# Kernel optimization log

Hardware: AMD Instinct MI355X
Metric: run time of the kernel (lower is better)

The kernel has to match this reference:

```python
import jax, jax.numpy as jnp
import numpy as np

HID = 128
N_NODES = 50000
N_EDGES = 640000
N_GRAPHS = 64
N_LAYERS = 3
LN_EPS = 1e-5


def _ln(h, g, b):
    mu = jnp.mean(h, axis=-1, keepdims=True)
    v = jnp.mean(jnp.square(h - mu), axis=-1, keepdims=True)
    return (h - mu) * jax.lax.rsqrt(v + LN_EPS) * g + b


def _mlp2(h, W1, b1, g, be, W2, b2):
    # Linear -> ReLU -> LayerNorm -> (Dropout=identity in eval) -> Linear
    h = _ln(jax.nn.relu(h @ W1.T + b1), g, be)
    return h @ W2.T + b2


def _forward(x, edge_index, batch, axis_W1, axis_b1, axis_g, axis_be, axis_W2, axis_b2, org_W1, org_b1, org_g, org_be, org_W2, org_b2, nin_W, nin_b, conv_W1, conv_b1, conv_g, conv_be, conv_W2, conv_b2, eps, ln_g, ln_b, gate_W1, gate_b1, gate_g, gate_be, gate_W2, gate_b2, head_W1, head_b1, head_g, head_be, head_W2, head_b2):
    axis = x[:, 9:12]
    origin = x[:, 12:15]
    others = jnp.concatenate([x[:, :9], x[:, 15:19]], axis=1)  # [N, 13]
    axis_z = _mlp2(axis, axis_W1, axis_b1, axis_g, axis_be, axis_W2, axis_b2)
    org_z = _mlp2(origin, org_W1, org_b1, org_g, org_be, org_W2, org_b2)
    h = jnp.concatenate([others, axis_z, org_z], axis=1) @ nin_W.T + nin_b  # [N, HID]
    src, dst = edge_index[0], edge_index[1]
    n = x.shape[0]
    for l in range(N_LAYERS):
        res = h
        # GIN: sum-aggregate source features into targets (gather + scatter-add)
        agg = jax.ops.segment_sum(h[src], dst, num_segments=n)
        m = (1.0 + eps[l]) * h + agg
        m = _mlp2(m, conv_W1[l], conv_b1[l], conv_g[l], conv_be[l], conv_W2[l], conv_b2[l])
        h = _ln(jax.nn.relu(m), ln_g[l], ln_b[l]) + res
    # AttentionalAggregation: segment softmax over per-graph node gates
    gate = _mlp2(h, gate_W1, gate_b1, gate_g, gate_be, gate_W2, gate_b2)  # [N, 1]
    gmax = jax.ops.segment_max(gate, batch, num_segments=N_GRAPHS)
    e = jnp.exp(gate - gmax[batch])
    denom = jax.ops.segment_sum(e, batch, num_segments=N_GRAPHS)
    attn = e / denom[batch]
    g = jax.ops.segment_sum(attn * h, batch, num_segments=N_GRAPHS)  # [B, HID]
    logit = _mlp2(g, head_W1, head_b1, head_g, head_be, head_W2, head_b2)[:, 0]
    return logit


def setup_inputs() -> dict:
    key = jax.random.key(0)
    ks = iter(jax.random.split(key, 64))
    nk = lambda: next(ks)
    lin = lambda o, i: jax.random.normal(nk(), (o, i), jnp.float32) / np.float32(np.sqrt(i))
    lin3 = lambda L, o, i: jnp.stack([lin(o, i) for _ in range(L)])
    z = lambda *s: jnp.zeros(s, jnp.float32)
    o = lambda *s: jnp.ones(s, jnp.float32)
    inp = {}
    inp['x'] = jax.random.normal(nk(), (N_NODES, 19), jnp.float32)
    inp['edge_index'] = jax.random.randint(nk(), (2, N_EDGES), 0, N_NODES)
    inp['batch'] = jnp.sort(jax.random.randint(nk(), (N_NODES,), 0, N_GRAPHS))
    for p in ('axis', 'org'):
        inp[p + '_W1'] = lin(16, 3); inp[p + '_b1'] = z(16)
        inp[p + '_g'] = o(16); inp[p + '_be'] = z(16)
        inp[p + '_W2'] = lin(16, 16); inp[p + '_b2'] = z(16)
    inp['nin_W'] = lin(HID, 45); inp['nin_b'] = z(HID)
    inp['conv_W1'] = lin3(N_LAYERS, HID, HID); inp['conv_b1'] = z(N_LAYERS, HID)
    inp['conv_g'] = o(N_LAYERS, HID); inp['conv_be'] = z(N_LAYERS, HID)
    inp['conv_W2'] = lin3(N_LAYERS, HID, HID); inp['conv_b2'] = z(N_LAYERS, HID)
    inp['eps'] = z(N_LAYERS)
    inp['ln_g'] = o(N_LAYERS, HID); inp['ln_b'] = z(N_LAYERS, HID)
    for p in ('gate', 'head'):
        inp[p + '_W1'] = lin(HID // 2, HID); inp[p + '_b1'] = z(HID // 2)
        inp[p + '_g'] = o(HID // 2); inp[p + '_be'] = z(HID // 2)
        inp[p + '_W2'] = lin(1, HID // 2); inp[p + '_b2'] = z(1)
    return inp


def reference(x, edge_index, batch, axis_W1, axis_b1, axis_g, axis_be, axis_W2, axis_b2, org_W1, org_b1, org_g, org_be, org_W2, org_b2, nin_W, nin_b, conv_W1, conv_b1, conv_g, conv_be, conv_W2, conv_b2, eps, ln_g, ln_b, gate_W1, gate_b1, gate_g, gate_be, gate_W2, gate_b2, head_W1, head_b1, head_g, head_be, head_W2, head_b2):
    return _forward(x, edge_index, batch, axis_W1, axis_b1, axis_g, axis_be, axis_W2, axis_b2, org_W1, org_b1, org_g, org_be, org_W2, org_b2, nin_W, nin_b, conv_W1, conv_b1, conv_g, conv_be, conv_W2, conv_b2, eps, ln_g, ln_b, gate_W1, gate_b1, gate_g, gate_be, gate_W2, gate_b2, head_W1, head_b1, head_g, head_be, head_W2, head_b2)
```

## Files before the change

### kernel.cpp

```cpp
#include <hip/hip_runtime.h>

#define N_NODESC 50000
#define N_EDGESC 640000
#define N_GRAPHSC 64
#define HIDC 128
#define LN_EPSF 1e-5f
#define POOL_SPLIT 16
#define SCAN_NB 49
#define EGRID ((N_EDGESC + 255) / 256)
#define NGRID_GB ((N_NODESC + 255) / 256)
#define NGRID64 ((N_NODESC + 63) / 64)
#define PREP_ELEMS (8192 + 49152 + 49152)
#define WPREP_NB ((PREP_ELEMS + 255) / 256)

typedef short bf16x8 __attribute__((ext_vector_type(8)));
typedef float f32x4 __attribute__((ext_vector_type(4)));

static __device__ __forceinline__ unsigned ord_enc(float f) {
  unsigned u = __float_as_uint(f);
  return (u & 0x80000000u) ? ~u : (u | 0x80000000u);
}
static __device__ __forceinline__ float ord_dec(unsigned u) {
  return __uint_as_float((u & 0x80000000u) ? (u ^ 0x80000000u) : ~u);
}
static __device__ __forceinline__ unsigned short f2bf(float x) {
  unsigned u = __float_as_uint(x);
  u += 0x7fffu + ((u >> 16) & 1u);
  return (unsigned short)(u >> 16);
}
static __device__ __forceinline__ float bf2f(unsigned short b) {
  return __uint_as_float(((unsigned)b) << 16);
}

static __device__ __forceinline__ void mlp16(float in0, float in1, float in2,
    const float* __restrict__ W1, const float* __restrict__ b1,
    const float* __restrict__ g, const float* __restrict__ be,
    const float* __restrict__ W2, const float* __restrict__ b2,
    float* __restrict__ out) {
  float h[16];
  float s1 = 0.f, s2 = 0.f;
#pragma unroll
  for (int j = 0; j < 16; ++j) {
    float v = b1[j] + W1[j*3+0]*in0 + W1[j*3+1]*in1 + W1[j*3+2]*in2;
    v = fmaxf(v, 0.f);
    h[j] = v; s1 += v; s2 += v*v;
  }
  float mu = s1 * (1.f/16.f);
  float var = fmaxf(s2 * (1.f/16.f) - mu*mu, 0.f);
  float rs = rsqrtf(var + LN_EPSF);
  float z[16];
#pragma unroll
  for (int j = 0; j < 16; ++j) z[j] = (h[j]-mu)*rs*g[j] + be[j];
#pragma unroll
  for (int j = 0; j < 16; ++j) {
    float v = b2[j];
#pragma unroll
    for (int k = 0; k < 16; ++k) v += W2[j*16+k]*z[k];
    out[j] = v;
  }
}

__global__ __launch_bounds__(256) void hist_gbound_kernel(const int* __restrict__ ei,
    int* __restrict__ deg, const int* __restrict__ batch, int* __restrict__ gstart,
    const float* __restrict__ ninW, unsigned short* __restrict__ ninWb,
    const float* __restrict__ cW1, unsigned short* __restrict__ cW1b,
    const float* __restrict__ cW2, unsigned short* __restrict__ cW2b) {
  const int b = blockIdx.x;
  if (b < EGRID) {
    int e = b * 256 + threadIdx.x;
    if (e < N_EDGESC) atomicAdd(&deg[ei[N_EDGESC + e]], 1);
  } else if (b < EGRID + NGRID_GB) {
    int i = (b - EGRID) * 256 + threadIdx.x;
    if (i >= N_NODESC) return;
    int bb = batch[i];
    int prev = (i == 0) ? -1 : batch[i-1];
    for (int g = prev + 1; g <= bb; ++g) gstart[g] = i;
    if (i == N_NODESC - 1) {
      for (int g = bb + 1; g <= N_GRAPHSC; ++g) gstart[g] = N_NODESC;
    }
  } else {
    int i = (b - EGRID - NGRID_GB) * 256 + threadIdx.x;
    if (i < 8192) {
      int f = i >> 6, k = i & 63;
      ninWb[i] = (k < 45) ? f2bf(ninW[f*45 + k]) : (unsigned short)0;
    } else if (i < 8192 + 49152) {
      int j = i - 8192;
      cW1b[j] = f2bf(cW1[j]);
    } else if (i < PREP_ELEMS) {
      int j = i - 8192 - 49152;
      cW2b[j] = f2bf(cW2[j]);
    }
  }
}

__global__ __launch_bounds__(1024) void scan1_kernel(const int* __restrict__ deg,
                                                     int* __restrict__ incl,
                                                     int* __restrict__ bsum) {
  const int b = blockIdx.x, t = threadIdx.x;
  const int i = b * 1024 + t;
  const int lane = t & 63, w = t >> 6;
  int v = (i < N_NODESC) ? deg[i] : 0;
#pragma unroll
  for (int off = 1; off < 64; off <<= 1) {
    int n = __shfl_up(v, off);
    if (lane >= off) v += n;
  }
  __shared__ int wsum[16];
  if (lane == 63) wsum[w] = v;
  __syncthreads();
  if (t == 0) {
    int run = 0;
#pragma unroll
    for (int k = 0; k < 16; ++k) { int x = wsum[k]; wsum[k] = run; run += x; }
  }
  __syncthreads();
  v += wsum[w];
  if (i < N_NODESC) incl[i] = v;
  if (t == 1023) bsum[b] = v;
}

__global__ __launch_bounds__(1024) void scan23_kernel(const int* __restrict__ deg,
                                                      const int* __restrict__ bsum,
                                                      int* __restrict__ rowptr,
                                                      int* __restrict__ cursor) {
  __shared__ int ex[SCAN_NB + 1];
  const int b = blockIdx.x, t = threadIdx.x;
  if (t < 64) {
    int v = (t < SCAN_NB) ? bsum[t] : 0;
    const int orig = v;
#pragma unroll
    for (int off = 1; off < 64; off <<= 1) {
      int n = __shfl_up(v, off);
      if (t >= off) v += n;
    }
    if (t < SCAN_NB) ex[t] = v - orig;
    if (t == SCAN_NB - 1) ex[SCAN_NB] = v;
  }
  __syncthreads();
  const int i = b * 1024 + t;
  if (i < N_NODESC) {
    int excl = rowptr[i] - deg[i] + ex[b];
    rowptr[i] = excl;
    cursor[i] = excl;
  }
  if (b == 0 && t == 0) rowptr[N_NODESC] = ex[SCAN_NB];
}

__global__ __launch_bounds__(256, 4) void scatter_enc_kernel(
    const int* __restrict__ ei, int* __restrict__ cursor, int* __restrict__ esrc,
    const float* __restrict__ x,
    const float* __restrict__ aW1, const float* __restrict__ ab1,
    const float* __restrict__ ag,  const float* __restrict__ abe,
    const float* __restrict__ aW2, const float* __restrict__ ab2,
    const float* __restrict__ oW1, const float* __restrict__ ob1,
    const float* __restrict__ og,  const float* __restrict__ obe,
    const float* __restrict__ oW2, const float* __restrict__ ob2,
    const unsigned short* __restrict__ ninWb, const float* __restrict__ ninb,
    unsigned short* __restrict__ Hb) {
  __shared__ unsigned short Ab[64*136];
  const int t = threadIdx.x;

  if (blockIdx.x >= NGRID64) {
    int e = (blockIdx.x - NGRID64) * 256 + t;
    if (e < N_EDGESC) {
      int d = ei[N_EDGESC + e];
      int slot = atomicAdd(&cursor[d], 1);
      esrc[slot] = ei[e];
    }
    return;
  }

  const int nb = blockIdx.x * 64;

  if (t < 192) {
    const int n = t & 63;
    const int gn = nb + n;
    const int grp = t >> 6;
    if (gn < N_NODESC) {
      const float* xr = x + gn * 19;
      if (grp == 0) {
        float z[16];
        mlp16(xr[9], xr[10], xr[11], aW1, ab1, ag, abe, aW2, ab2, z);
#pragma unroll
        for (int k = 0; k < 16; ++k) Ab[n*136 + 13 + k] = f2bf(z[k]);
      } else if (grp == 1) {
        float z[16];
        mlp16(xr[12], xr[13], xr[14], oW1, ob1, og, obe, oW2, ob2, z);
#pragma unroll
        for (int k = 0; k < 16; ++k) Ab[n*136 + 29 + k] = f2bf(z[k]);
      } else {
#pragma unroll
        for (int k = 0; k < 9; ++k) Ab[n*136 + k] = f2bf(xr[k]);
#pragma unroll
        for (int k = 0; k < 4; ++k) Ab[n*136 + 9 + k] = f2bf(xr[15 + k]);
#pragma unroll
        for (int k = 45; k < 64; ++k) Ab[n*136 + k] = 0;
      }
    } else {
      if (grp == 0) {
#pragma unroll
        for (int k = 0; k < 16; ++k) Ab[n*136 + 13 + k] = 0;
      } else if (grp == 1) {
#pragma unroll
        for (int k = 0; k < 16; ++k) Ab[n*136 + 29 + k] = 0;
      } else {
#pragma unroll
        for (int k = 0; k < 13; ++k) Ab[n*136 + k] = 0;
#pragma unroll
        for (int k = 45; k < 64; ++k) Ab[n*136 + k] = 0;
      }
    }
  }
  __syncthreads();

  const int lane = t & 63, wv = t >> 6;
  const int quad = lane >> 4, l16 = lane & 15;
  const int arow = (wv*16 + l16)*136 + quad*8;
  f32x4 acc[8];
#pragma unroll
  for (int ft = 0; ft < 8; ++ft) acc[ft] = (f32x4){0.f,0.f,0.f,0.f};
#pragma unroll
  for (int ks = 0; ks < 2; ++ks) {
    bf16x8 a = *(const bf16x8*)(const void*)&Ab[arow + ks*32];
#pragma unroll
    for (int ft = 0; ft < 8; ++ft) {
      bf16x8 bfr = *(const bf16x8*)&ninWb[(ft*16 + l16)*64 + quad*8 + ks*32];
      acc[ft] = __builtin_amdgcn_mfma_f32_16x16x32_bf16(a, bfr, acc[ft], 0, 0, 0);
    }
  }
  float bb[8];
#pragma unroll
  for (int ft = 0; ft < 8; ++ft) bb[ft] = ninb[ft*16 + l16];
  __syncthreads();
#pragma unroll
  for (int r = 0; r < 4; ++r) {
    int nloc = wv*16 + quad*4 + r;
#pragma unroll
    for (int ft = 0; ft < 8; ++ft)
      Ab[nloc*136 + ft*16 + l16] = f2bf(acc[ft][r] + bb[ft]);
  }
  __syncthreads();
#pragma unroll
  for (int i = 0; i < 4; ++i) {
    int chunk = t + i*256;
    int n = chunk >> 4, c8 = chunk & 15;
    int gn = nb + n;
    if (gn < N_NODESC)
      *(bf16x8*)&Hb[gn*HIDC + c8*8] = *(const bf16x8*)&Ab[n*136 + c8*8];
  }
}

template<bool GATE>
__global__ __launch_bounds__(256, 3) void layer_kernel(
    const unsigned short* __restrict__ Hin,
    const int* __restrict__ rowptr, const int* __restrict__ esrc,
    const float* __restrict__ epsp,
    const unsigned short* __restrict__ W1b, const float* __restrict__ b1,
    const float* __restrict__ g1, const float* __restrict__ be1,
    const unsigned short* __restrict__ W2b, const float* __restrict__ b2,
    const float* __restrict__ lng, const float* __restrict__ lnb,
    unsigned short* __restrict__ Hout,
    const float* __restrict__ gW1, const float* __restrict__ gb1,
    const float* __restrict__ glng, const float* __restrict__ glnb,
    const float* __restrict__ gW2, const float* __restrict__ gb2,
    const int* __restrict__ batch, float* __restrict__ gateb,
    unsigned* __restrict__ gmaxu) {
  __shared__ unsigned short Ab[64*136];
  __shared__ unsigned short Wl[128*136];
  __shared__ unsigned sgm[N_GRAPHSC];
  const int t = threadIdx.x;
  const int nb = blockIdx.x * 64;
  if (GATE && t < N_GRAPHSC) sgm[t] = 0u;

#pragma unroll
  for (int i = 0; i < 8; ++i) {
    int q = t + i*256;
    int f = q >> 4, cc = q & 15;
    *(bf16x8*)&Wl[f*136 + cc*8] = *(const bf16x8*)&W1b[f*HIDC + cc*8];
  }

  {
    const float e1 = 1.0f + epsp[0];
    const int c8 = t & 15;
    const int nv = t >> 4;
#pragma unroll
    for (int p = 0; p < 4; ++p) {
      const int n = p*16 + nv;
      const int gn = nb + n;
      bf16x8 m8 = {0,0,0,0,0,0,0,0};
      if (gn < N_NODESC) {
        bf16x8 h = *(const bf16x8*)&Hin[gn*HIDC + c8*8];
        float acc[8];
#pragma unroll
        for (int k = 0; k < 8; ++k) acc[k] = 0.f;
        int s = rowptr[gn];
        const int e = rowptr[gn+1];
        for (; s + 4 <= e; s += 4) {
          int i0 = esrc[s], i1 = esrc[s+1], i2 = esrc[s+2], i3 = esrc[s+3];
          bf16x8 x0 = *(const bf16x8*)&Hin[i0*HIDC + c8*8];
          bf16x8 x1 = *(const bf16x8*)&Hin[i1*HIDC + c8*8];
          bf16x8 x2 = *(const bf16x8*)&Hin[i2*HIDC + c8*8];
          bf16x8 x3 = *(const bf16x8*)&Hin[i3*HIDC + c8*8];
#pragma unroll
          for (int k = 0; k < 8; ++k)
            acc[k] += (bf2f((unsigned short)x0[k]) + bf2f((unsigned short)x1[k]))
                    + (bf2f((unsigned short)x2[k]) + bf2f((unsigned short)x3[k]));
        }
        for (; s < e; ++s) {
          bf16x8 x0 = *(const bf16x8*)&Hin[esrc[s]*HIDC + c8*8];
#pragma unroll
          for (int k = 0; k < 8; ++k) acc[k] += bf2f((unsigned short)x0[k]);
        }
#pragma unroll
        for (int k = 0; k < 8; ++k)
          m8[k] = (short)f2bf(e1*bf2f((unsigned short)h[k]) + acc[k]);
      }
      *(bf16x8*)&Ab[n*136 + c8*8] = m8;
    }
  }
  __syncthreads();

  const int lane = t & 63, wv = t >> 6;
  const int quad = lane >> 4, l16 = lane & 15;
  const int arow = (wv*16 + l16)*136 + quad*8;

  f32x4 acc[8];
#pragma unroll
  for (int ft = 0; ft < 8; ++ft) acc[ft] = (f32x4){0.f,0.f,0.f,0.f};
#pragma unroll
  for (int ks = 0; ks < 4; ++ks) {
    bf16x8 a = *(const bf16x8*)(const void*)&Ab[arow + ks*32];
#pragma unroll
    for (int ft = 0; ft < 8; ++ft) {
      bf16x8 b = *(const bf16x8*)(const void*)&Wl[(ft*16 + l16)*136 + quad*8 + ks*32];
      acc[ft] = __builtin_amdgcn_mfma_f32_16x16x32_bf16(a, b, acc[ft], 0, 0, 0);
    }
  }

  {
    float bb[8], gg[8], bee[8];
#pragma unroll
    for (int ft = 0; ft < 8; ++ft) {
      int f = ft*16 + l16;
      bb[ft] = b1[f]; gg[ft] = g1[f]; bee[ft] = be1[f];
    }
    float s1[4] = {0,0,0,0}, s2[4] = {0,0,0,0};
#pragma unroll
    for (int ft = 0; ft < 8; ++ft)
#pragma unroll
      for (int r = 0; r < 4; ++r) {
        float v = fmaxf(acc[ft][r] + bb[ft], 0.f);
        acc[ft][r] = v; s1[r] += v; s2[r] += v*v;
      }
#pragma unroll
    for (int m = 1; m < 16; m <<= 1)
#pragma unroll
      for (int r = 0; r < 4; ++r) {
        s1[r] += __shfl_xor(s1[r], m);
        s2[r] += __shfl_xor(s2[r], m);
      }
    float mu[4], rs[4];
#pragma unroll
    for (int r = 0; r < 4; ++r) {
      mu[r] = s1[r] * (1.f/128.f);
      float var = fmaxf(s2[r] * (1.f/128.f) - mu[r]*mu[r], 0.f);
      rs[r] = rsqrtf(var + LN_EPSF);
    }
    __syncthreads();
#pragma unroll
    for (int r = 0; r < 4; ++r) {
      int nloc = wv*16 + quad*4 + r;
#pragma unroll
      for (int ft = 0; ft < 8; ++ft) {
        float o = (acc[ft][r] - mu[r])*rs[r]*gg[ft] + bee[ft];
        Ab[nloc*136 + ft*16 + l16] = f2bf(o);
      }
    }
  }
#pragma unroll
  for (int i = 0; i < 8; ++i) {
    int q = t + i*256;
    int f = q >> 4, cc = q & 15;
    *(bf16x8*)&Wl[f*136 + cc*8] = *(const bf16x8*)&W2b[f*HIDC + cc*8];
  }
  __syncthreads();

#pragma unroll
  for (int ft = 0; ft < 8; ++ft) acc[ft] = (f32x4){0.f,0.f,0.f,0.f};
#pragma unroll
  for (int ks = 0; ks < 4; ++ks) {
    bf16x8 a = *(const bf16x8*)(const void*)&Ab[arow + ks*32];
#pragma unroll
    for (int ft = 0; ft < 8; ++ft) {
      bf16x8 b = *(const bf16x8*)(const void*)&Wl[(ft*16 + l16)*136 + quad*8 + ks*32];
      acc[ft] = __builtin_amdgcn_mfma_f32_16x16x32_bf16(a, b, acc[ft], 0, 0, 0);
    }
  }

  {
    float bb[8], gg[8], bee[8];
#pragma unroll
    for (int ft = 0; ft < 8; ++ft) {
      int f = ft*16 + l16;
      bb[ft] = b2[f]; gg[ft] = lng[f]; bee[ft] = lnb[f];
    }
    float s1[4] = {0,0,0,0}, s2[4] = {0,0,0,0};
#pragma unroll
    for (int ft = 0; ft < 8; ++ft)
#pragma unroll
      for (int r = 0; r < 4; ++r) {
        float v = fmaxf(acc[ft][r] + bb[ft], 0.f);
        acc[ft][r] = v; s1[r] += v; s2[r] += v*v;
      }
#pragma unroll
    for (int m = 1; m < 16; m <<= 1)
#pragma unroll
      for (int r = 0; r < 4; ++r) {
        s1[r] += __shfl_xor(s1[r], m);
        s2[r] += __shfl_xor(s2[r], m);
      }
    float mu[4], rs[4];
#pragma unroll
    for (int r = 0; r < 4; ++r) {
      mu[r] = s1[r] * (1.f/128.f);
      float var = fmaxf(s2[r] * (1.f/128.f) - mu[r]*mu[r], 0.f);
      rs[r] = rsqrtf(var + LN_EPSF);
    }
    __syncthreads();
#pragma unroll
    for (int r = 0; r < 4; ++r) {
      int nloc = wv*16 + quad*4 + r;
#pragma unroll
      for (int ft = 0; ft < 8; ++ft) {
        float o = (acc[ft][r] - mu[r])*rs[r]*gg[ft] + bee[ft];
        Ab[nloc*136 + ft*16 + l16] = f2bf(o);
      }
    }
  }
  __syncthreads();
#pragma unroll
  for (int i = 0; i < 4; ++i) {
    int chunk = t + i*256;
    int n = chunk >> 4, cc = chunk & 15;
    int gn = nb + n;
    bf16x8 o8 = {0,0,0,0,0,0,0,0};
    if (gn < N_NODESC) {
      bf16x8 vv = *(const bf16x8*)&Ab[n*136 + cc*8];
      bf16x8 rr = *(const bf16x8*)&Hin[gn*HIDC + cc*8];
#pragma unroll
      for (int k = 0; k < 8; ++k)
        o8[k] = (short)f2bf(bf2f((unsigned short)vv[k]) + bf2f((unsigned short)rr[k]));
      *(bf16x8*)&Hout[gn*HIDC + cc*8] = o8;
    }
    if (GATE) *(bf16x8*)&Ab[n*136 + cc*8] = o8;
  }

  if (GATE) {
#pragma unroll
    for (int i = 0; i < 8; ++i) {
      int q = t + i*256;
      int f = q >> 5, c4 = q & 31;
      float4 v = *(const float4*)&gW1[f*HIDC + c4*4];
      ushort4 hh;
      hh.x = f2bf(v.x); hh.y = f2bf(v.y); hh.z = f2bf(v.z); hh.w = f2bf(v.w);
      *(ushort4*)&Wl[f*136 + c4*4] = hh;
    }
    __syncthreads();

    f32x4 gacc[4];
#pragma unroll
    for (int ft = 0; ft < 4; ++ft) gacc[ft] = (f32x4){0.f,0.f,0.f,0.f};
#pragma unroll
    for (int ks = 0; ks < 4; ++ks) {
      bf16x8 a = *(const bf16x8*)(const void*)&Ab[arow + ks*32];
#pragma unroll
      for (int ft = 0; ft < 4; ++ft) {
        bf16x8 b = *(const bf16x8*)(const void*)&Wl[(ft*16 + l16)*136 + quad*8 + ks*32];
        gacc[ft] = __builtin_amdgcn_mfma_f32_16x16x32_bf16(a, b, gacc[ft], 0, 0, 0);
      }
    }

    float bb[4], gg[4], bee[4], w2v[4];
#pragma unroll
    for (int ft = 0; ft < 4; ++ft) {
      int f = ft*16 + l16;
      bb[ft] = gb1[f]; gg[ft] = glng[f]; bee[ft] = glnb[f]; w2v[ft] = gW2[f];
    }
    float s1[4] = {0,0,0,0}, s2[4] = {0,0,0,0};
#pragma unroll
    for (int ft = 0; ft < 4; ++ft)
#pragma unroll
      for (int r = 0; r < 4; ++r) {
        float v = fmaxf(gacc[ft][r] + bb[ft], 0.f);
        gacc[ft][r] = v; s1[r] += v; s2[r] += v*v;
      }
#pragma unroll
    for (int m = 1; m < 16; m <<= 1)
#pragma unroll
      for (int r = 0; r < 4; ++r) {
        s1[r] += __shfl_xor(s1[r], m);
        s2[r] += __shfl_xor(s2[r], m);
      }
    float pd[4];
#pragma unroll
    for (int r = 0; r < 4; ++r) {
      float mu = s1[r] * (1.f/64.f);
      float var = fmaxf(s2[r] * (1.f/64.f) - mu*mu, 0.f);
      float rs = rsqrtf(var + LN_EPSF);
      float p = 0.f;
#pragma unroll
      for (int ft = 0; ft < 4; ++ft)
        p += ((gacc[ft][r] - mu)*rs*gg[ft] + bee[ft]) * w2v[ft];
      pd[r] = p;
    }
#pragma unroll
    for (int m = 1; m < 16; m <<= 1)
#pragma unroll
      for (int r = 0; r < 4; ++r) pd[r] += __shfl_xor(pd[r], m);
    if (l16 == 0) {
      float b2v = gb2[0];
#pragma unroll
      for (int r = 0; r < 4; ++r) {
        int node = nb + wv*16 + quad*4 + r;
        if (node < N_NODESC) {
          float gv = pd[r] + b2v;
          gateb[node] = gv;
          atomicMax(&sgm[batch[node]], ord_enc(gv));
        }
      }
    }
    __syncthreads();
    if (t < N_GRAPHSC && sgm[t] != 0u) atomicMax(&gmaxu[t], sgm[t]);
  }
}

__global__ __launch_bounds__(256) void pool_kernel(const unsigned short* __restrict__ Hb,
    const float* __restrict__ gateb, const int* __restrict__ gstart,
    const unsigned* __restrict__ gmaxu, float* __restrict__ S,
    float* __restrict__ denom) {
  const int g    = blockIdx.x / POOL_SPLIT;
  const int part = blockIdx.x % POOL_SPLIT;
  const int s0 = gstart[g], s1 = gstart[g+1];
  const int cnt = s1 - s0;
  const int chunk = (cnt + POOL_SPLIT - 1) / POOL_SPLIT;
  int lo = s0 + part * chunk;
  int hi = lo + chunk; if (hi > s1) hi = s1;
  const int t = threadIdx.x;
  const int c8 = t & 15;
  const int v  = t >> 4;
  const float gm = ord_dec(gmaxu[g]);
  float acc[8];
#pragma unroll
  for (int k = 0; k < 8; ++k) acc[k] = 0.f;
  float de = 0.f;
  for (int n = lo + v; n < hi; n += 16) {
    float e = expf(gateb[n] - gm);
    bf16x8 hv = *(const bf16x8*)&Hb[n*HIDC + c8*8];
#pragma unroll
    for (int k = 0; k < 8; ++k) acc[k] += e * bf2f((unsigned short)hv[k]);
    if (c8 == 0) de += e;
  }
  __shared__ float sacc[16*128];
  __shared__ float sden[16];
#pragma unroll
  for (int k = 0; k < 8; ++k) sacc[v*128 + c8*8 + k] = acc[k];
  if (c8 == 0) sden[v] = de;
  __syncthreads();
  if (t < 128) {
    float s = 0.f;
#pragma unroll
    for (int vv = 0; vv < 16; ++vv) s += sacc[vv*128 + t];
    atomicAdd(&S[g*HIDC + t], s);
  }
  if (t == 0) {
    float d = 0.f;
#pragma unroll
    for (int vv = 0; vv < 16; ++vv) d += sden[vv];
    atomicAdd(&denom[g], d);
  }
}

__global__ __launch_bounds__(64) void head_kernel(const float* __restrict__ S,
    const float* __restrict__ denom, const float* __restrict__ W1,
    const float* __restrict__ b1, const float* __restrict__ g,
    const float* __restrict__ be, const float* __restrict__ W2,
    const float* __restrict__ b2, float* __restrict__ out) {
  const int gr = blockIdx.x;
  const int j = threadIdx.x;
  const float inv = 1.0f / denom[gr];
  float v = b1[j];
  for (int k = 0; k < HIDC; ++k) v += (S[gr*HIDC + k] * inv) * W1[j*HIDC + k];
  v = fmaxf(v, 0.f);
  float s1 = v, s2 = v*v;
  for (int off = 32; off; off >>= 1) { s1 += __shfl_xor(s1, off); s2 += __shfl_xor(s2, off); }
  float mu = s1 * (1.f/64.f);
  float var = fmaxf(s2 * (1.f/64.f) - mu*mu, 0.f);
  float rs = rsqrtf(var + LN_EPSF);
  float z = (v-mu)*rs*g[j] + be[j];
  float p = z * W2[j];
  for (int off = 32; off; off >>= 1) p += __shfl_xor(p, off);
  if (j == 0) out[gr] = p + b2[0];
}

extern "C" void kernel_launch(void* const* d_in, const int* in_sizes, int n_in,
                              void* d_out, int out_size, void* d_ws, size_t ws_size,
                              hipStream_t stream) {
  (void)in_sizes; (void)n_in; (void)out_size; (void)ws_size;
  const float* x     = (const float*)d_in[0];
  const int*   ei    = (const int*)d_in[1];
  const int*   batch = (const int*)d_in[2];
  const float* aW1 = (const float*)d_in[3];
  const float* ab1 = (const float*)d_in[4];
  const float* ag  = (const float*)d_in[5];
  const float* abe = (const float*)d_in[6];
  const float* aW2 = (const float*)d_in[7];
  const float* ab2 = (const float*)d_in[8];
  const float* oW1 = (const float*)d_in[9];
  const float* ob1 = (const float*)d_in[10];
  const float* og  = (const float*)d_in[11];
  const float* obe = (const float*)d_in[12];
  const float* oW2 = (const float*)d_in[13];
  const float* ob2 = (const float*)d_in[14];
  const float* ninW = (const float*)d_in[15];
  const float* ninb = (const float*)d_in[16];
  const float* cW1 = (const float*)d_in[17];
  const float* cb1 = (const float*)d_in[18];
  const float* cg  = (const float*)d_in[19];
  const float* cbe = (const float*)d_in[20];
  const float* cW2 = (const float*)d_in[21];
  const float* cb2 = (const float*)d_in[22];
  const float* eps = (const float*)d_in[23];
  const float* lng = (const float*)d_in[24];
  const float* lnb = (const float*)d_in[25];
  const float* gW1 = (const float*)d_in[26];
  const float* gb1 = (const float*)d_in[27];
  const float* gg  = (const float*)d_in[28];
  const float* gbe = (const float*)d_in[29];
  const float* gW2 = (const float*)d_in[30];
  const float* gb2 = (const float*)d_in[31];
  const float* hW1 = (const float*)d_in[32];
  const float* hb1 = (const float*)d_in[33];
  const float* hg  = (const float*)d_in[34];
  const float* hbe = (const float*)d_in[35];
  const float* hW2 = (const float*)d_in[36];
  const float* hb2 = (const float*)d_in[37];

  char* ws = (char*)d_ws;
  unsigned short* Ha = (unsigned short*)(ws + 0);
  unsigned short* Hc = (unsigned short*)(ws + 12800000);
  float* gateb = (float*)(ws + 38400000);
  int*   deg   = (int*)(ws + 38600000);
  float* S     = (float*)(ws + 38800000);
  float* denom = (float*)(ws + 38832768);
  unsigned* gmaxu = (unsigned*)(ws + 38833024);
  int* rowptr  = (int*)(ws + 38833280);
  int* cursor  = (int*)(ws + 39033284);
  int* esrc    = (int*)(ws + 39233284);
  int* bsum    = (int*)(ws + 41793284);
  int* gstart  = (int*)(ws + 41793540);
  unsigned short* ninWb = (unsigned short*)(ws + 41800000);
  unsigned short* cW1b  = (unsigned short*)(ws + 41816384);
  unsigned short* cW2b  = (unsigned short*)(ws + 41914688);

  hipMemsetAsync(deg, 0, 233280, stream);

  hist_gbound_kernel<<<EGRID + NGRID_GB + WPREP_NB, 256, 0, stream>>>(
      ei, deg, batch, gstart, ninW, ninWb, cW1, cW1b, cW2, cW2b);
  scan1_kernel<<<SCAN_NB, 1024, 0, stream>>>(deg, rowptr, bsum);
  scan23_kernel<<<SCAN_NB, 1024, 0, stream>>>(deg, bsum, rowptr, cursor);
  scatter_enc_kernel<<<NGRID64 + EGRID, 256, 0, stream>>>(
      ei, cursor, esrc,
      x, aW1, ab1, ag, abe, aW2, ab2,
      oW1, ob1, og, obe, oW2, ob2,
      ninWb, ninb, Ha);

  layer_kernel<false><<<NGRID64, 256, 0, stream>>>(
      Ha, rowptr, esrc, eps + 0,
      cW1b + 0*HIDC*HIDC, cb1 + 0*HIDC, cg + 0*HIDC, cbe + 0*HIDC,
      cW2b + 0*HIDC*HIDC, cb2 + 0*HIDC, lng + 0*HIDC, lnb + 0*HIDC,
      Hc,
      gW1, gb1, gg, gbe, gW2, gb2, batch, gateb, gmaxu);
  layer_kernel<false><<<NGRID64, 256, 0, stream>>>(
      Hc, rowptr, esrc, eps + 1,
      cW1b + 1*HIDC*HIDC, cb1 + 1*HIDC, cg + 1*HIDC, cbe + 1*HIDC,
      cW2b + 1*HIDC*HIDC, cb2 + 1*HIDC, lng + 1*HIDC, lnb + 1*HIDC,
      Ha,
      gW1, gb1, gg, gbe, gW2, gb2, batch, gateb, gmaxu);
  layer_kernel<true><<<NGRID64, 256, 0, stream>>>(
      Ha, rowptr, esrc, eps + 2,
      cW1b + 2*HIDC*HIDC, cb1 + 2*HIDC, cg + 2*HIDC, cbe + 2*HIDC,
      cW2b + 2*HIDC*HIDC, cb2 + 2*HIDC, lng + 2*HIDC, lnb + 2*HIDC,
      Hc,
      gW1, gb1, gg, gbe, gW2, gb2, batch, gateb, gmaxu);

  pool_kernel<<<N_GRAPHSC * POOL_SPLIT, 256, 0, stream>>>(Hc, gateb, gstart, gmaxu, S, denom);
  head_kernel<<<N_GRAPHSC, 64, 0, stream>>>(S, denom, hW1, hb1, hg, hbe, hW2, hb2,
                                            (float*)d_out);
}
```

Baseline: 405.6 us.

## Split neighbor aggregation out of fused GIN layer kernel into separate kernel

Each GIN layer's gather and sum aggregation moves out of the GEMM-pair kernel into its own lightweight kernel with 128-thread blocks of 8 nodes, which writes the aggregated message to a workspace buffer. The GEMM kernel then just loads that buffer into shared memory. The aim is to stop the latency-bound irregular gather from running in a kernel whose occupancy is limited by large shared memory and MFMA register use, so the gather gets more parallelism. The cost is an extra round trip of a node-sized bf16 buffer through global memory and one more kernel launch per layer.

```diff
diff --git a/kernel.cpp b/kernel.cpp
--- a/kernel.cpp
+++ b/kernel.cpp
@@ -250,11 +250,48 @@
   }
 }
 
+__global__ __launch_bounds__(128) void agg_kernel(const unsigned short* __restrict__ Hb,
+    const int* __restrict__ rowptr, const int* __restrict__ esrc,
+    const float* __restrict__ epsp, unsigned short* __restrict__ Mb) {
+  const int t = threadIdx.x;
+  const int c8 = t & 15;
+  const int v  = t >> 4;
+  const int node = blockIdx.x * 8 + v;
+  if (node >= N_NODESC) return;
+  const float e1 = 1.0f + epsp[0];
+  bf16x8 h = *(const bf16x8*)&Hb[node*HIDC + c8*8];
+  float acc[8];
+#pragma unroll
+  for (int k = 0; k < 8; ++k) acc[k] = 0.f;
+  int s = rowptr[node];
+  const int e = rowptr[node+1];
+  for (; s + 4 <= e; s += 4) {
+    int i0 = esrc[s], i1 = esrc[s+1], i2 = esrc[s+2], i3 = esrc[s+3];
+    bf16x8 x0 = *(const bf16x8*)&Hb[i0*HIDC + c8*8];
+    bf16x8 x1 = *(const bf16x8*)&Hb[i1*HIDC + c8*8];
+    bf16x8 x2 = *(const bf16x8*)&Hb[i2*HIDC + c8*8];
+    bf16x8 x3 = *(const bf16x8*)&Hb[i3*HIDC + c8*8];
+#pragma unroll
+    for (int k = 0; k < 8; ++k)
+      acc[k] += (bf2f((unsigned short)x0[k]) + bf2f((unsigned short)x1[k]))
+              + (bf2f((unsigned short)x2[k]) + bf2f((unsigned short)x3[k]));
+  }
+  for (; s < e; ++s) {
+    bf16x8 x0 = *(const bf16x8*)&Hb[esrc[s]*HIDC + c8*8];
+#pragma unroll
+    for (int k = 0; k < 8; ++k) acc[k] += bf2f((unsigned short)x0[k]);
+  }
+  bf16x8 m8;
+#pragma unroll
+  for (int k = 0; k < 8; ++k)
+    m8[k] = (short)f2bf(e1*bf2f((unsigned short)h[k]) + acc[k]);
+  *(bf16x8*)&Mb[node*HIDC + c8*8] = m8;
+}
+
 template<bool GATE>
-__global__ __launch_bounds__(256, 3) void layer_kernel(
+__global__ __launch_bounds__(256, 3) void gemmpair_kernel(
+    const unsigned short* __restrict__ Mb,
     const unsigned short* __restrict__ Hin,
-    const int* __restrict__ rowptr, const int* __restrict__ esrc,
-    const float* __restrict__ epsp,
     const unsigned short* __restrict__ W1b, const float* __restrict__ b1,
     const float* __restrict__ g1, const float* __restrict__ be1,
     const unsigned short* __restrict__ W2b, const float* __restrict__ b2,
@@ -273,50 +310,19 @@
   if (GATE && t < N_GRAPHSC) sgm[t] = 0u;
 
 #pragma unroll
+  for (int i = 0; i < 4; ++i) {
+    int chunk = t + i*256;
+    int n = chunk >> 4, c8 = chunk & 15;
+    int gn = nb + n;
+    bf16x8 v = {0,0,0,0,0,0,0,0};
+    if (gn < N_NODESC) v = *(const bf16x8*)&Mb[gn*HIDC + c8*8];
+    *(bf16x8*)&Ab[n*136 + c8*8] = v;
+  }
+#pragma unroll
   for (int i = 0; i < 8; ++i) {
     int q = t + i*256;
-    int f = q >> 4, cc = q & 15;
-    *(bf16x8*)&Wl[f*136 + cc*8] = *(const bf16x8*)&W1b[f*HIDC + cc*8];
-  }
-
-  {
-    const float e1 = 1.0f + epsp[0];
-    const int c8 = t & 15;
-    const int nv = t >> 4;
-#pragma unroll
-    for (int p = 0; p < 4; ++p) {
-      const int n = p*16 + nv;
-      const int gn = nb + n;
-      bf16x8 m8 = {0,0,0,0,0,0,0,0};
-      if (gn < N_NODESC) {
-        bf16x8 h = *(const bf16x8*)&Hin[gn*HIDC + c8*8];
-        float acc[8];
-#pragma unroll
-        for (int k = 0; k < 8; ++k) acc[k] = 0.f;
-        int s = rowptr[gn];
-        const int e = rowptr[gn+1];
-        for (; s + 4 <= e; s += 4) {
-          int i0 = esrc[s], i1 = esrc[s+1], i2 = esrc[s+2], i3 = esrc[s+3];
-          bf16x8 x0 = *(const bf16x8*)&Hin[i0*HIDC + c8*8];
-          bf16x8 x1 = *(const bf16x8*)&Hin[i1*HIDC + c8*8];
-          bf16x8 x2 = *(const bf16x8*)&Hin[i2*HIDC + c8*8];
-          bf16x8 x3 = *(const bf16x8*)&Hin[i3*HIDC + c8*8];
-#pragma unroll
-          for (int k = 0; k < 8; ++k)
-            acc[k] += (bf2f((unsigned short)x0[k]) + bf2f((unsigned short)x1[k]))
-                    + (bf2f((unsigned short)x2[k]) + bf2f((unsigned short)x3[k]));
-        }
-        for (; s < e; ++s) {
-          bf16x8 x0 = *(const bf16x8*)&Hin[esrc[s]*HIDC + c8*8];
-#pragma unroll
-          for (int k = 0; k < 8; ++k) acc[k] += bf2f((unsigned short)x0[k]);
-        }
-#pragma unroll
-        for (int k = 0; k < 8; ++k)
-          m8[k] = (short)f2bf(e1*bf2f((unsigned short)h[k]) + acc[k]);
-      }
-      *(bf16x8*)&Ab[n*136 + c8*8] = m8;
-    }
+    int f = q >> 4, c8 = q & 15;
+    *(bf16x8*)&Wl[f*136 + c8*8] = *(const bf16x8*)&W1b[f*HIDC + c8*8];
   }
   __syncthreads();
 
@@ -380,8 +386,8 @@
 #pragma unroll
   for (int i = 0; i < 8; ++i) {
     int q = t + i*256;
-    int f = q >> 4, cc = q & 15;
-    *(bf16x8*)&Wl[f*136 + cc*8] = *(const bf16x8*)&W2b[f*HIDC + cc*8];
+    int f = q >> 4, c8 = q & 15;
+    *(bf16x8*)&Wl[f*136 + c8*8] = *(const bf16x8*)&W2b[f*HIDC + c8*8];
   }
   __syncthreads();
 
@@ -648,6 +654,7 @@
   char* ws = (char*)d_ws;
   unsigned short* Ha = (unsigned short*)(ws + 0);
   unsigned short* Hc = (unsigned short*)(ws + 12800000);
+  unsigned short* Mb = (unsigned short*)(ws + 25600000);
   float* gateb = (float*)(ws + 38400000);
   int*   deg   = (int*)(ws + 38600000);
   float* S     = (float*)(ws + 38800000);
@@ -674,24 +681,27 @@
       oW1, ob1, og, obe, oW2, ob2,
       ninWb, ninb, Ha);
 
-  layer_kernel<false><<<NGRID64, 256, 0, stream>>>(
-      Ha, rowptr, esrc, eps + 0,
-      cW1b + 0*HIDC*HIDC, cb1 + 0*HIDC, cg + 0*HIDC, cbe + 0*HIDC,
-      cW2b + 0*HIDC*HIDC, cb2 + 0*HIDC, lng + 0*HIDC, lnb + 0*HIDC,
-      Hc,
-      gW1, gb1, gg, gbe, gW2, gb2, batch, gateb, gmaxu);
-  layer_kernel<false><<<NGRID64, 256, 0, stream>>>(
-      Hc, rowptr, esrc, eps + 1,
-      cW1b + 1*HIDC*HIDC, cb1 + 1*HIDC, cg + 1*HIDC, cbe + 1*HIDC,
-      cW2b + 1*HIDC*HIDC, cb2 + 1*HIDC, lng + 1*HIDC, lnb + 1*HIDC,
-      Ha,
-      gW1, gb1, gg, gbe, gW2, gb2, batch, gateb, gmaxu);
-  layer_kernel<true><<<NGRID64, 256, 0, stream>>>(
-      Ha, rowptr, esrc, eps + 2,
-      cW1b + 2*HIDC*HIDC, cb1 + 2*HIDC, cg + 2*HIDC, cbe + 2*HIDC,
-      cW2b + 2*HIDC*HIDC, cb2 + 2*HIDC, lng + 2*HIDC, lnb + 2*HIDC,
-      Hc,
-      gW1, gb1, gg, gbe, gW2, gb2, batch, gateb, gmaxu);
+  unsigned short* cur = Ha;
+  unsigned short* nxt = Hc;
+  for (int l = 0; l < 3; ++l) {
+    agg_kernel<<<(N_NODESC + 7) / 8, 128, 0, stream>>>(cur, rowptr, esrc, eps + l, Mb);
+    if (l < 2) {
+      gemmpair_kernel<false><<<NGRID64, 256, 0, stream>>>(
+          Mb, cur,
+          cW1b + l*HIDC*HIDC, cb1 + l*HIDC, cg + l*HIDC, cbe + l*HIDC,
+          cW2b + l*HIDC*HIDC, cb2 + l*HIDC, lng + l*HIDC, lnb + l*HIDC,
+          nxt,
+          gW1, gb1, gg, gbe, gW2, gb2, batch, gateb, gmaxu);
+    } else {
+      gemmpair_kernel<true><<<NGRID64, 256, 0, stream>>>(
+          Mb, cur,
+          cW1b + l*HIDC*HIDC, cb1 + l*HIDC, cg + l*HIDC, cbe + l*HIDC,
+          cW2b + l*HIDC*HIDC, cb2 + l*HIDC, lng + l*HIDC, lnb + l*HIDC,
+          nxt,
+          gW1, gb1, gg, gbe, gW2, gb2, batch, gateb, gmaxu);
+    }
+    unsigned short* tmp = cur; cur = nxt; nxt = tmp;
+  }
 
   pool_kernel<<<N_GRAPHSC * POOL_SPLIT, 256, 0, stream>>>(Hc, gateb, gstart, gmaxu, S, denom);
   head_kernel<<<N_GRAPHSC, 64, 0, stream>>>(S, denom, hW1, hb1, hg, hbe, hW2, hb2,
```

Measured after the change: 373.3 us. 8.0% less time.
